# Performance work log

Measured on AMD Instinct MI355X. Metric: run time of the kernel, lower is better.

The kernel has to match this reference:

```python
import jax, jax.numpy as jnp
import numpy as np

B, S, H, NH = 2, 2048, 1024, 16
D = H // NH

def setup_inputs() -> dict:
    key = jax.random.key(0)
    ks = jax.random.split(key, 9)
    s = 1.0 / np.sqrt(H)
    return {
        "x": jax.random.normal(ks[0], (B, S, H), jnp.float32),
        "wq": jax.random.uniform(ks[1], (H, H), jnp.float32, -s, s),
        "bq": jax.random.uniform(ks[2], (H,), jnp.float32, -s, s),
        "wk": jax.random.uniform(ks[3], (H, H), jnp.float32, -s, s),
        "bk": jax.random.uniform(ks[4], (H,), jnp.float32, -s, s),
        "wv": jax.random.uniform(ks[5], (H, H), jnp.float32, -s, s),
        "bv": jax.random.uniform(ks[6], (H,), jnp.float32, -s, s),
        "wo": jax.random.uniform(ks[7], (H, H), jnp.float32, -s, s),
        "bo": jax.random.uniform(ks[8], (H,), jnp.float32, -s, s),
    }

def _split_heads(t):
    # [B, S, H] -> [B, NH, S, D]
    return t.reshape(B, S, NH, D).transpose(0, 2, 1, 3)

def reference(x, wq, bq, wk, bk, wv, bv, wo, bo):
    q = _split_heads(x @ wq.T + bq)
    k = _split_heads(x @ wk.T + bk)
    v = _split_heads(x @ wv.T + bv)
    scores = jnp.einsum('bhqd,bhkd->bhqk', q, k) / jnp.sqrt(jnp.float32(D))
    attn = jax.nn.softmax(scores, axis=-1)  # full [B,NH,S,S] materialized as in source
    ctx = jnp.einsum('bhqk,bhkd->bhqd', attn, v)
    concat = ctx.transpose(0, 2, 1, 3).reshape(B, S, H)
    return concat @ wo.T + bo
```

## Files before the change

kernel.cpp:

```cpp
#include <hip/hip_runtime.h>
#include <cstdint>

typedef unsigned short u16;
typedef __attribute__((ext_vector_type(8))) short short8;
typedef __attribute__((ext_vector_type(4))) float f32x4;

#if __has_builtin(__builtin_amdgcn_exp2f)
#define EXP2F(x) __builtin_amdgcn_exp2f(x)
#else
#define EXP2F(x) exp2f(x)
#endif

__device__ inline u16 f2bf(float f) {
  union { float f; unsigned u; } v; v.f = f;
  unsigned u = v.u;
  return (u16)((u + 0x7fffu + ((u >> 16) & 1u)) >> 16);
}

__device__ inline unsigned pk2bf_fast(float a, float b) {
  union { float f; unsigned u; } ua, ub; ua.f = a; ub.f = b;
  return __builtin_amdgcn_perm(ub.u + 0x8000u, ua.u + 0x8000u, 0x07060302u);
}

__device__ inline void gl2lds16(const void* g, void* l) {
  __builtin_amdgcn_global_load_lds(
      (const __attribute__((address_space(1))) unsigned int*)(unsigned long long)(uintptr_t)g,
      (__attribute__((address_space(3))) unsigned int*)(unsigned int)(uintptr_t)l,
      16, 0, 0);
}


__global__ __launch_bounds__(256) void cvt_kernel(
    const float* __restrict__ x,
    const float* __restrict__ wq, const float* __restrict__ wk,
    const float* __restrict__ wv, const float* __restrict__ wo,
    u16* __restrict__ xb, u16* __restrict__ wqb, u16* __restrict__ wkb,
    u16* __restrict__ wvb, u16* __restrict__ wob) {
  const int y = blockIdx.y;
  const int Q = 1 << 20;
  const float* src;
  u16* dst;
  if (y < 4)       { src = x + y * Q; dst = xb + y * Q; }
  else if (y == 4) { src = wq; dst = wqb; }
  else if (y == 5) { src = wk; dst = wkb; }
  else if (y == 6) { src = wv; dst = wvb; }
  else             { src = wo; dst = wob; }
  const int i = (blockIdx.x * 256 + threadIdx.x) * 8;
  float4 a = *(const float4*)(src + i);
  float4 b = *(const float4*)(src + i + 4);
  short8 o;
  o[0] = (short)f2bf(a.x); o[1] = (short)f2bf(a.y);
  o[2] = (short)f2bf(a.z); o[3] = (short)f2bf(a.w);
  o[4] = (short)f2bf(b.x); o[5] = (short)f2bf(b.y);
  o[6] = (short)f2bf(b.z); o[7] = (short)f2bf(b.w);
  const int j = (i & ~63) | (((((i >> 3) & 7) ^ ((i >> 10) & 7))) << 3);
  *(short8*)(dst + j) = o;
}

__global__ __launch_bounds__(256, 2) void gemm_qkv(
    const u16* __restrict__ xb,
    const u16* __restrict__ wqb, const u16* __restrict__ wkb, const u16* __restrict__ wvb,
    const float* __restrict__ bq, const float* __restrict__ bk, const float* __restrict__ bv,
    u16* __restrict__ qo, u16* __restrict__ ko, u16* __restrict__ vto) {
  __shared__ u16 smem[40960];
  u16* As = smem;
  u16* Bs = smem + 16384;
  const int tid = threadIdx.x, lane = tid & 63;
  const int wid = tid >> 6;
  const int l15 = lane & 15, lg = lane >> 4;
  const int m0 = blockIdx.y * 128, n0 = blockIdx.x * 64;
  const int sw = ((l15 & 7) << 3);
  const u16* Wz[3] = {wqb, wkb, wvb};

  f32x4 acc[3][2][4] = {};

#pragma unroll
  for (int i = 0; i < 4; ++i) {
    int c = i * 256 + tid;
    gl2lds16(xb + (m0 + (c >> 3)) * 1024 + (c & 7) * 8, As + c * 8);
  }
#pragma unroll
  for (int z = 0; z < 3; ++z)
#pragma unroll
    for (int i = 0; i < 2; ++i) {
      int c = i * 256 + tid;
      gl2lds16(Wz[z] + (n0 + (c >> 3)) * 1024 + (c & 7) * 8, Bs + z * 4096 + c * 8);
    }

  for (int k0 = 0; k0 < 1024; k0 += 64) {
    const int p = (k0 >> 6) & 1;
    __syncthreads();
    if (k0 < 960) {
      u16* An = As + (1 - p) * 8192;
      u16* Bn = Bs + (1 - p) * 12288;
#pragma unroll
      for (int i = 0; i < 4; ++i) {
        int c = i * 256 + tid;
        gl2lds16(xb + (m0 + (c >> 3)) * 1024 + k0 + 64 + (c & 7) * 8, An + c * 8);
      }
#pragma unroll
      for (int z = 0; z < 3; ++z)
#pragma unroll
        for (int i = 0; i < 2; ++i) {
          int c = i * 256 + tid;
          gl2lds16(Wz[z] + (n0 + (c >> 3)) * 1024 + k0 + 64 + (c & 7) * 8, Bn + z * 4096 + c * 8);
        }
    }
    const u16* Ap = As + p * 8192;
    const u16* Bp = Bs + p * 12288;
#pragma unroll
    for (int kk = 0; kk < 2; ++kk) {
      short8 af[2], bf[3][4];
#pragma unroll
      for (int mb = 0; mb < 2; ++mb)
        af[mb] = *(const short8*)(Ap + (wid * 32 + mb * 16 + l15) * 64 + ((((kk * 4 + lg) << 3)) ^ sw));
#pragma unroll
      for (int z = 0; z < 3; ++z)
#pragma unroll
        for (int nb = 0; nb < 4; ++nb)
          bf[z][nb] = *(const short8*)(Bp + z * 4096 + (nb * 16 + l15) * 64 + ((((kk * 4 + lg) << 3)) ^ sw));
#pragma unroll
      for (int z = 0; z < 3; ++z)
#pragma unroll
        for (int mb = 0; mb < 2; ++mb)
#pragma unroll
          for (int nb = 0; nb < 4; ++nb)
            acc[z][mb][nb] = __builtin_amdgcn_mfma_f32_16x16x32_bf16(af[mb], bf[z][nb], acc[z][mb][nb], 0, 0, 0);
    }
  }

  const float cexp = 0.18033688011112042f;

#pragma unroll
  for (int mb = 0; mb < 2; ++mb)
#pragma unroll
    for (int nb = 0; nb < 4; ++nb)
#pragma unroll
      for (int r = 0; r < 4; ++r) {
        int m = m0 + wid * 32 + mb * 16 + lg * 4 + r;
        int n = n0 + nb * 16 + l15;
        float v = (acc[0][mb][nb][r] + bq[n]) * cexp;
        int b = m >> 11, s = m & 2047, hh = n >> 6, d = n & 63;
        qo[((b * 16 + hh) * 2048 + s) * 64 + d] = f2bf(v);
      }

#pragma unroll
  for (int mb = 0; mb < 2; ++mb)
#pragma unroll
    for (int nb = 0; nb < 4; ++nb)
#pragma unroll
      for (int r = 0; r < 4; ++r) {
        int m = m0 + wid * 32 + mb * 16 + lg * 4 + r;
        int n = n0 + nb * 16 + l15;
        float v = acc[1][mb][nb][r] + bk[n];
        int b = m >> 11, s = m & 2047, hh = n >> 6, d = n & 63;
        int dcol = (((d >> 3) ^ (s & 7)) << 3) | (d & 7);
        ko[((b * 16 + hh) * 2048 + s) * 64 + dcol] = f2bf(v);
      }

  __syncthreads();
  {
    u16* wbuf = smem + (wid >> 1) * 4608;
    const int so = (wid & 1) * 2;
#pragma unroll
    for (int mb = 0; mb < 2; ++mb)
#pragma unroll
      for (int nb = 0; nb < 4; ++nb) {
        int n = n0 + nb * 16 + l15;
        float bn = bv[n];
        int dl = nb * 16 + l15;
#pragma unroll
        for (int r = 0; r < 4; ++r) {
          int sig = (lg * 4 + r) * 4 + so + mb;
          wbuf[dl * 72 + sig] = f2bf(acc[2][mb][nb][r] + bn);
        }
      }
    __syncthreads();
    int hh = n0 >> 6;
    int bb = m0 >> 11;
    int sbase = m0 & 2047;
#pragma unroll
    for (int i = 0; i < 4; ++i) {
      int idx = i * 256 + tid;
      int p2 = idx >> 9, rem = idx & 511;
      int dl = rem >> 3, c = rem & 7;
      short8 vv = *(const short8*)(smem + p2 * 4608 + dl * 72 + c * 8);
      int cs = c ^ (dl & 7);
      *(short8*)(vto + ((bb * 16 + hh) * 64 + dl) * 2048 + sbase + p2 * 64 + cs * 8) = vv;
    }
  }
}

__global__ __launch_bounds__(256, 2) void attn_kernel(
    const u16* __restrict__ qg, const u16* __restrict__ kg,
    const u16* __restrict__ vtg, u16* __restrict__ ctxg) {
  const int h = blockIdx.x, qt = blockIdx.y, b = blockIdx.z;
  const int bh = b * 16 + h;
  const u16* Qg = qg + (bh * 2048 + qt * 128) * 64;
  const u16* Kg = kg + bh * 2048 * 64;
  const u16* Vg = vtg + bh * 64 * 2048;

  __shared__ u16 SP[128 * 72];
  __shared__ u16 KV[2][8192];

  const int tid = threadIdx.x, lane = tid & 63, wid = tid >> 6;
  const int l15 = lane & 15, lg = lane >> 4;
  const int row0 = wid * 32;
  const int sw = ((l15 & 7) << 3);

  short8 qf[2][2];
#pragma unroll
  for (int mb = 0; mb < 2; ++mb)
#pragma unroll
    for (int kk = 0; kk < 2; ++kk)
      qf[mb][kk] = *(const short8*)(Qg + (row0 + mb * 16 + l15) * 64 + kk * 32 + lg * 8);

  short8 ones8;
#pragma unroll
  for (int j = 0; j < 8; ++j) ones8[j] = (short)0x3F80;

#pragma unroll
  for (int i = 0; i < 2; ++i) {
    int c = i * 256 + tid;
    gl2lds16(Kg + c * 8, &KV[0][c * 8]);
    gl2lds16(Vg + (c >> 3) * 2048 + (c & 7) * 8, &KV[0][4096 + c * 8]);
  }

  f32x4 acc[2][5] = {};

  for (int kt = 0; kt < 32; ++kt) {
    const int p = kt & 1;
    __syncthreads();
    if (kt < 31) {
#pragma unroll
      for (int i = 0; i < 2; ++i) {
        int c = i * 256 + tid;
        gl2lds16(Kg + (kt + 1) * 4096 + c * 8, &KV[1 - p][c * 8]);
        gl2lds16(Vg + (c >> 3) * 2048 + (kt + 1) * 64 + (c & 7) * 8, &KV[1 - p][4096 + c * 8]);
      }
    }
    const u16* Ks = &KV[p][0];
    const u16* Vts = &KV[p][4096];

    f32x4 sc[2][4] = {};
#pragma unroll
    for (int kk = 0; kk < 2; ++kk) {
      short8 bfr[4];
#pragma unroll
      for (int nb = 0; nb < 4; ++nb)
        bfr[nb] = *(const short8*)(Ks + (nb * 16 + l15) * 64 + ((((kk * 4 + lg) << 3)) ^ sw));
#pragma unroll
      for (int mb = 0; mb < 2; ++mb)
#pragma unroll
        for (int nb = 0; nb < 4; ++nb)
          sc[mb][nb] = __builtin_amdgcn_mfma_f32_16x16x32_bf16(qf[mb][kk], bfr[nb], sc[mb][nb], 0, 0, 0);
    }

#pragma unroll
    for (int mb = 0; mb < 2; ++mb)
#pragma unroll
      for (int r = 0; r < 4; ++r) {
        float p0 = EXP2F(sc[mb][0][r]);
        float p1 = EXP2F(sc[mb][1][r]);
        float p2 = EXP2F(sc[mb][2][r]);
        float p3 = EXP2F(sc[mb][3][r]);
        uint2 u;
        u.x = pk2bf_fast(p0, p1);
        u.y = pk2bf_fast(p2, p3);
        *(uint2*)(SP + (row0 + mb * 16 + lg * 4 + r) * 72 + l15 * 4) = u;
      }

#pragma unroll
    for (int kk = 0; kk < 2; ++kk) {
      short8 pa[2], vb[4];
#pragma unroll
      for (int mb = 0; mb < 2; ++mb)
        pa[mb] = *(const short8*)(SP + (row0 + mb * 16 + l15) * 72 + kk * 32 + lg * 8);
#pragma unroll
      for (int nd = 0; nd < 4; ++nd)
        vb[nd] = *(const short8*)(Vts + (nd * 16 + l15) * 64 + ((((kk * 4 + lg) << 3)) ^ sw));
#pragma unroll
      for (int mb = 0; mb < 2; ++mb) {
#pragma unroll
        for (int nd = 0; nd < 4; ++nd)
          acc[mb][nd] = __builtin_amdgcn_mfma_f32_16x16x32_bf16(pa[mb], vb[nd], acc[mb][nd], 0, 0, 0);
        acc[mb][4] = __builtin_amdgcn_mfma_f32_16x16x32_bf16(pa[mb], ones8, acc[mb][4], 0, 0, 0);
      }
    }
  }

#pragma unroll
  for (int mb = 0; mb < 2; ++mb)
#pragma unroll
    for (int r = 0; r < 4; ++r) {
      float inv = 1.0f / acc[mb][4][r];
      int s = qt * 128 + row0 + mb * 16 + lg * 4 + r;
      int s7 = s & 7;
      u16* dst = ctxg + (b * 2048 + s) * 1024 + h * 64;
#pragma unroll
      for (int nd = 0; nd < 4; ++nd) {
        int d = nd * 16 + l15;
        int dcol = (((d >> 3) ^ s7) << 3) | (d & 7);
        dst[dcol] = f2bf(acc[mb][nd][r] * inv);
      }
    }
}

__global__ __launch_bounds__(256) void gemm_out(
    const u16* __restrict__ cb, const u16* __restrict__ wob,
    const float* __restrict__ bo, float* __restrict__ out) {
  __shared__ u16 smem[16384];
  u16* As = smem;
  u16* Bs = smem + 8192;
  const int tid = threadIdx.x, lane = tid & 63;
  const int wid = tid >> 6;
  const int l15 = lane & 15, lg = lane >> 4;
  const int m0 = blockIdx.y * 64, n0 = blockIdx.x * 64;
  const int sw = ((l15 & 7) << 3);

  f32x4 acc[4] = {};

#pragma unroll
  for (int i = 0; i < 2; ++i) {
    int c = i * 256 + tid;
    gl2lds16(cb  + (m0 + (c >> 3)) * 1024 + (c & 7) * 8, As + c * 8);
    gl2lds16(wob + (n0 + (c >> 3)) * 1024 + (c & 7) * 8, Bs + c * 8);
  }

  for (int k0 = 0; k0 < 1024; k0 += 64) {
    const int p = (k0 >> 6) & 1;
    __syncthreads();
    if (k0 < 960) {
      u16* An = As + (1 - p) * 4096;
      u16* Bn = Bs + (1 - p) * 4096;
#pragma unroll
      for (int i = 0; i < 2; ++i) {
        int c = i * 256 + tid;
        gl2lds16(cb  + (m0 + (c >> 3)) * 1024 + k0 + 64 + (c & 7) * 8, An + c * 8);
        gl2lds16(wob + (n0 + (c >> 3)) * 1024 + k0 + 64 + (c & 7) * 8, Bn + c * 8);
      }
    }
    const u16* Ap = As + p * 4096;
    const u16* Bp = Bs + p * 4096;
#pragma unroll
    for (int kk = 0; kk < 2; ++kk) {
      short8 af, bf[4];
      af = *(const short8*)(Ap + (wid * 16 + l15) * 64 + ((((kk * 4 + lg) << 3)) ^ sw));
#pragma unroll
      for (int nb = 0; nb < 4; ++nb)
        bf[nb] = *(const short8*)(Bp + (nb * 16 + l15) * 64 + ((((kk * 4 + lg) << 3)) ^ sw));
#pragma unroll
      for (int nb = 0; nb < 4; ++nb)
        acc[nb] = __builtin_amdgcn_mfma_f32_16x16x32_bf16(af, bf[nb], acc[nb], 0, 0, 0);
    }
  }

#pragma unroll
  for (int nb = 0; nb < 4; ++nb)
#pragma unroll
    for (int r = 0; r < 4; ++r) {
      int m = m0 + wid * 16 + lg * 4 + r;
      int n = n0 + nb * 16 + l15;
      out[m * 1024 + n] = acc[nb][r] + bo[n];
    }
}

extern "C" void kernel_launch(void* const* d_in, const int* in_sizes, int n_in,
                              void* d_out, int out_size, void* d_ws, size_t ws_size,
                              hipStream_t stream) {
  const float* x  = (const float*)d_in[0];
  const float* wq = (const float*)d_in[1];
  const float* bq = (const float*)d_in[2];
  const float* wk = (const float*)d_in[3];
  const float* bk = (const float*)d_in[4];
  const float* wv = (const float*)d_in[5];
  const float* bv = (const float*)d_in[6];
  const float* wo = (const float*)d_in[7];
  const float* bo = (const float*)d_in[8];

  if (ws_size < (size_t)24 * 1024 * 1024 * 2) return;
  u16* xb   = (u16*)d_ws;
  u16* wqb  = xb  + (4u << 20);
  u16* wkb  = wqb + (1u << 20);
  u16* wvb  = wkb + (1u << 20);
  u16* wob  = wvb + (1u << 20);
  u16* qb   = wob + (1u << 20);
  u16* kb   = qb  + (4u << 20);
  u16* vtb  = kb  + (4u << 20);
  u16* ctxb = vtb + (4u << 20);

  cvt_kernel<<<dim3(512, 8, 1), 256, 0, stream>>>(x, wq, wk, wv, wo, xb, wqb, wkb, wvb, wob);
  gemm_qkv<<<dim3(16, 32, 1), 256, 0, stream>>>(xb, wqb, wkb, wvb, bq, bk, bv, qb, kb, vtb);
  attn_kernel<<<dim3(16, 16, 2), 256, 0, stream>>>(qb, kb, vtb, ctxb);
  gemm_out<<<dim3(16, 64, 1), 256, 0, stream>>>(ctxb, wob, bo, (float*)d_out);
}
```

Before: 180.3 us.

## Compute transposed S^T in attention to keep P in registers, skipping LDS round-trip

The attention kernel now computes scores as K·Q^T so that the MFMA output layout directly matches the B-operand layout for the P·V product, letting the exp'd probabilities stay in registers instead of being written to and reread from shared memory. The V projection's staging index is permuted to match the new key ordering expected by the register-resident P fragments. The output context is staged through LDS and written with 16-byte vector stores instead of scattered 2-byte stores. This removes per-tile LDS traffic and a write-read dependency, at the cost of a subtle layout coupling between the QKV kernel's V layout and the attention kernel.

Result: faster. 169.9 us (-5.8%).

```diff
diff --git a/kernel.cpp b/kernel.cpp
--- a/kernel.cpp
+++ b/kernel.cpp
@@ -4,6 +4,7 @@
 typedef unsigned short u16;
 typedef __attribute__((ext_vector_type(8))) short short8;
 typedef __attribute__((ext_vector_type(4))) float f32x4;
+typedef __attribute__((ext_vector_type(4))) unsigned short ushort4v;
 
 #if __has_builtin(__builtin_amdgcn_exp2f)
 #define EXP2F(x) __builtin_amdgcn_exp2f(x)
@@ -161,7 +162,6 @@
   __syncthreads();
   {
     u16* wbuf = smem + (wid >> 1) * 4608;
-    const int so = (wid & 1) * 2;
 #pragma unroll
     for (int mb = 0; mb < 2; ++mb)
 #pragma unroll
@@ -171,7 +171,7 @@
         int dl = nb * 16 + l15;
 #pragma unroll
         for (int r = 0; r < 4; ++r) {
-          int sig = (lg * 4 + r) * 4 + so + mb;
+          int sig = (wid & 1) * 32 + lg * 8 + mb * 4 + r;
           wbuf[dl * 72 + sig] = f2bf(acc[2][mb][nb][r] + bn);
         }
       }
@@ -210,10 +210,10 @@
 
   short8 qf[2][2];
 #pragma unroll
-  for (int mb = 0; mb < 2; ++mb)
+  for (int qtile = 0; qtile < 2; ++qtile)
 #pragma unroll
     for (int kk = 0; kk < 2; ++kk)
-      qf[mb][kk] = *(const short8*)(Qg + (row0 + mb * 16 + l15) * 64 + kk * 32 + lg * 8);
+      qf[qtile][kk] = *(const short8*)(Qg + (row0 + qtile * 16 + l15) * 64 + kk * 32 + lg * 8);
 
   short8 ones8;
 #pragma unroll
@@ -226,7 +226,8 @@
     gl2lds16(Vg + (c >> 3) * 2048 + (c & 7) * 8, &KV[0][4096 + c * 8]);
   }
 
-  f32x4 acc[2][5] = {};
+  f32x4 acc[4][2] = {};
+  f32x4 accl[2] = {};
 
   for (int kt = 0; kt < 32; ++kt) {
     const int p = kt & 1;
@@ -242,68 +243,75 @@
     const u16* Ks = &KV[p][0];
     const u16* Vts = &KV[p][4096];
 
-    f32x4 sc[2][4] = {};
+    f32x4 sc[4][2] = {};
 #pragma unroll
     for (int kk = 0; kk < 2; ++kk) {
-      short8 bfr[4];
-#pragma unroll
-      for (int nb = 0; nb < 4; ++nb)
-        bfr[nb] = *(const short8*)(Ks + (nb * 16 + l15) * 64 + ((((kk * 4 + lg) << 3)) ^ sw));
-#pragma unroll
-      for (int mb = 0; mb < 2; ++mb)
-#pragma unroll
-        for (int nb = 0; nb < 4; ++nb)
-          sc[mb][nb] = __builtin_amdgcn_mfma_f32_16x16x32_bf16(qf[mb][kk], bfr[nb], sc[mb][nb], 0, 0, 0);
-    }
-
-#pragma unroll
-    for (int mb = 0; mb < 2; ++mb)
-#pragma unroll
-      for (int r = 0; r < 4; ++r) {
-        float p0 = EXP2F(sc[mb][0][r]);
-        float p1 = EXP2F(sc[mb][1][r]);
-        float p2 = EXP2F(sc[mb][2][r]);
-        float p3 = EXP2F(sc[mb][3][r]);
-        uint2 u;
-        u.x = pk2bf_fast(p0, p1);
-        u.y = pk2bf_fast(p2, p3);
-        *(uint2*)(SP + (row0 + mb * 16 + lg * 4 + r) * 72 + l15 * 4) = u;
-      }
-
-#pragma unroll
-    for (int kk = 0; kk < 2; ++kk) {
-      short8 pa[2], vb[4];
-#pragma unroll
-      for (int mb = 0; mb < 2; ++mb)
-        pa[mb] = *(const short8*)(SP + (row0 + mb * 16 + l15) * 72 + kk * 32 + lg * 8);
-#pragma unroll
-      for (int nd = 0; nd < 4; ++nd)
-        vb[nd] = *(const short8*)(Vts + (nd * 16 + l15) * 64 + ((((kk * 4 + lg) << 3)) ^ sw));
-#pragma unroll
-      for (int mb = 0; mb < 2; ++mb) {
-#pragma unroll
-        for (int nd = 0; nd < 4; ++nd)
-          acc[mb][nd] = __builtin_amdgcn_mfma_f32_16x16x32_bf16(pa[mb], vb[nd], acc[mb][nd], 0, 0, 0);
-        acc[mb][4] = __builtin_amdgcn_mfma_f32_16x16x32_bf16(pa[mb], ones8, acc[mb][4], 0, 0, 0);
-      }
-    }
-  }
-
-#pragma unroll
-  for (int mb = 0; mb < 2; ++mb)
-#pragma unroll
-    for (int r = 0; r < 4; ++r) {
-      float inv = 1.0f / acc[mb][4][r];
-      int s = qt * 128 + row0 + mb * 16 + lg * 4 + r;
-      int s7 = s & 7;
-      u16* dst = ctxg + (b * 2048 + s) * 1024 + h * 64;
-#pragma unroll
-      for (int nd = 0; nd < 4; ++nd) {
-        int d = nd * 16 + l15;
-        int dcol = (((d >> 3) ^ s7) << 3) | (d & 7);
-        dst[dcol] = f2bf(acc[mb][nd][r] * inv);
-      }
-    }
+      short8 kf[4];
+#pragma unroll
+      for (int ktile = 0; ktile < 4; ++ktile)
+        kf[ktile] = *(const short8*)(Ks + (ktile * 16 + l15) * 64 + ((((kk * 4 + lg) << 3)) ^ sw));
+#pragma unroll
+      for (int ktile = 0; ktile < 4; ++ktile)
+#pragma unroll
+        for (int qtile = 0; qtile < 2; ++qtile)
+          sc[ktile][qtile] = __builtin_amdgcn_mfma_f32_16x16x32_bf16(kf[ktile], qf[qtile][kk], sc[ktile][qtile], 0, 0, 0);
+    }
+
+    short8 pf[2][2];
+#pragma unroll
+    for (int sl = 0; sl < 2; ++sl)
+#pragma unroll
+      for (int qtile = 0; qtile < 2; ++qtile) {
+        union { short8 s; unsigned u[4]; } pu;
+        float a0 = EXP2F(sc[sl * 2][qtile][0]),     a1 = EXP2F(sc[sl * 2][qtile][1]);
+        float a2 = EXP2F(sc[sl * 2][qtile][2]),     a3 = EXP2F(sc[sl * 2][qtile][3]);
+        float b0 = EXP2F(sc[sl * 2 + 1][qtile][0]), b1 = EXP2F(sc[sl * 2 + 1][qtile][1]);
+        float b2 = EXP2F(sc[sl * 2 + 1][qtile][2]), b3 = EXP2F(sc[sl * 2 + 1][qtile][3]);
+        pu.u[0] = pk2bf_fast(a0, a1);
+        pu.u[1] = pk2bf_fast(a2, a3);
+        pu.u[2] = pk2bf_fast(b0, b1);
+        pu.u[3] = pk2bf_fast(b2, b3);
+        pf[sl][qtile] = pu.s;
+      }
+
+#pragma unroll
+    for (int sl = 0; sl < 2; ++sl) {
+      short8 vf[4];
+#pragma unroll
+      for (int dtile = 0; dtile < 4; ++dtile)
+        vf[dtile] = *(const short8*)(Vts + (dtile * 16 + l15) * 64 + ((((sl * 4 + lg) << 3)) ^ sw));
+#pragma unroll
+      for (int dtile = 0; dtile < 4; ++dtile)
+#pragma unroll
+        for (int qtile = 0; qtile < 2; ++qtile)
+          acc[dtile][qtile] = __builtin_amdgcn_mfma_f32_16x16x32_bf16(vf[dtile], pf[sl][qtile], acc[dtile][qtile], 0, 0, 0);
+#pragma unroll
+      for (int qtile = 0; qtile < 2; ++qtile)
+        accl[qtile] = __builtin_amdgcn_mfma_f32_16x16x32_bf16(ones8, pf[sl][qtile], accl[qtile], 0, 0, 0);
+    }
+  }
+
+#pragma unroll
+  for (int qtile = 0; qtile < 2; ++qtile) {
+    float inv = 1.0f / accl[qtile][0];
+#pragma unroll
+    for (int dtile = 0; dtile < 4; ++dtile) {
+      ushort4v pk;
+#pragma unroll
+      for (int r = 0; r < 4; ++r)
+        pk[r] = f2bf(acc[dtile][qtile][r] * inv);
+      *(ushort4v*)(SP + (row0 + qtile * 16 + l15) * 72 + dtile * 16 + lg * 4) = pk;
+    }
+  }
+#pragma unroll
+  for (int i = 0; i < 4; ++i) {
+    int idx = i * 64 + lane;
+    int rl = idx >> 3, c = idx & 7;
+    short8 vv = *(const short8*)(SP + (row0 + rl) * 72 + c * 8);
+    int s = qt * 128 + row0 + rl;
+    int cs = c ^ (s & 7);
+    *(short8*)(ctxg + ((long)b * 2048 + s) * 1024 + h * 64 + cs * 8) = vv;
+  }
 }
 
 __global__ __launch_bounds__(256) void gemm_out(
```
